# Optimization experiments

Measured on AMD Instinct MI355X. Metric: run time of the kernel, lower is better.

## Reference

```python
import jax, jax.numpy as jnp
import numpy as np

B, T, D = 2, 2048, 2048
H = 16
HD = D // H  # 128


def _rotate_half(x):
    x1, x2 = x[..., :HD // 2], x[..., HD // 2:]
    return jnp.concatenate((-x2, x1), axis=-1)


def setup_inputs() -> dict:
    key = jax.random.key(0)
    ks = jax.random.split(key, 7)
    return {
        "x": jax.random.normal(ks[0], (B, T, D), dtype=jnp.float32),
        "rope_cos": jax.random.uniform(ks[1], (1, 1, T, HD), dtype=jnp.float32),
        "rope_sin": jax.random.uniform(ks[2], (1, 1, T, HD), dtype=jnp.float32),
        "qkv_w": jax.random.normal(ks[3], (3 * D, D), dtype=jnp.float32) * (1.0 / np.sqrt(D)),
        "qkv_b": jax.random.normal(ks[4], (3 * D,), dtype=jnp.float32) * 0.02,
        "out_w": jax.random.normal(ks[5], (D, D), dtype=jnp.float32) * (1.0 / np.sqrt(D)),
        "out_b": jax.random.normal(ks[6], (D,), dtype=jnp.float32) * 0.02,
    }


def reference(x, rope_cos, rope_sin, qkv_w, qkv_b, out_w, out_b):
    bsz, t, d = x.shape
    # fused QKV projection (torch Linear: x @ W.T + b)
    qkv = x @ qkv_w.T + qkv_b                       # [B, T, 3D]
    qkv = qkv.reshape(bsz, t, 3, H, HD).transpose(2, 0, 3, 1, 4)  # [3, B, H, T, HD]
    q, k, v = qkv[0], qkv[1], qkv[2]
    # RoPE
    cos = rope_cos[:, :, :t, :]
    sin = rope_sin[:, :, :t, :]
    q = q * cos + _rotate_half(q) * sin
    k = k * cos + _rotate_half(k) * sin
    # causal SDPA (eval mode -> no dropout)
    scale = 1.0 / np.sqrt(HD)
    scores = jnp.einsum("bhqd,bhkd->bhqk", q, k) * scale
    causal = jnp.tril(jnp.ones((t, t), dtype=bool))
    scores = jnp.where(causal, scores, jnp.finfo(scores.dtype).min)
    attn = jax.nn.softmax(scores, axis=-1)
    out = jnp.einsum("bhqk,bhkd->bhqd", attn, v)    # [B, H, T, HD]
    out = out.transpose(0, 2, 1, 3).reshape(bsz, t, d)
    return out @ out_w.T + out_b
```

## Files before the change

### kernel.cpp

```cpp
#include <hip/hip_runtime.h>

typedef unsigned short u16;
typedef __attribute__((ext_vector_type(8))) short bf16x8;
typedef __attribute__((ext_vector_type(4))) float f32x4;

__device__ __forceinline__ float bf2f(unsigned int u) {
    union { unsigned int i; float f; } x; x.i = u << 16; return x.f;
}
__device__ __forceinline__ u16 f2bf(float f) {
    union { float f; unsigned int i; } x; x.f = f;
    unsigned int r = x.i + 0x7fffu + ((x.i >> 16) & 1u);
    return (u16)(r >> 16);
}

__device__ __forceinline__ void gl2lds16(const u16* g, u16* l) {
    __builtin_amdgcn_global_load_lds(
        (const __attribute__((address_space(1))) unsigned int*)g,
        (__attribute__((address_space(3))) unsigned int*)l, 16, 0, 0);
}

#define NX  8388608
#define NW1 12582912
#define NW2 4194304
__global__ __launch_bounds__(256) void convert_kernel(
    const float* __restrict__ x, const float* __restrict__ w1,
    const float* __restrict__ w2, u16* __restrict__ dst)
{
    const int i = (blockIdx.x * 256 + threadIdx.x) * 4;
    const float* src;
    int off;
    if (i < NX)            { src = x;  off = i; }
    else if (i < NX + NW1) { src = w1; off = i - NX; }
    else                   { src = w2; off = i - NX - NW1; }
    float4 v = *(const float4*)(src + off);
    ushort4 o;
    o.x = f2bf(v.x); o.y = f2bf(v.y); o.z = f2bf(v.z); o.w = f2bf(v.w);
    *(ushort4*)(dst + i) = o;
}

#define NTILES 64
#define BUFSZ  12288

#define GEMM_SETUP(Ag, Bg)                                                    \
    const int tid = threadIdx.x;                                              \
    const int wave = tid >> 6, lane = tid & 63;                               \
    const int l16 = lane & 15, quad = lane >> 4;                              \
    const int wr = wave >> 2, wc = wave & 3;                                  \
    f32x4 acc[4][4];                                                          \
    _Pragma("unroll") for (int mi = 0; mi < 4; ++mi)                          \
        _Pragma("unroll") for (int ni = 0; ni < 4; ++ni)                      \
            acc[mi][ni] = (f32x4){0.f, 0.f, 0.f, 0.f};                        \
    int aoff[4], boff[4];                                                     \
    _Pragma("unroll") for (int mi = 0; mi < 4; ++mi) {                        \
        const int r = wr * 64 + mi * 16 + l16;                                \
        aoff[mi] = r * 32 + ((quad ^ ((r >> 1) & 3)) << 3);                   \
    }                                                                         \
    _Pragma("unroll") for (int ni = 0; ni < 4; ++ni) {                        \
        const int r = (wc >> 1) * 128 + (ni >> 1) * 64 + (wc & 1) * 32        \
                    + (ni & 1) * 16 + l16;                                    \
        boff[ni] = 4096 + r * 32 + ((quad ^ ((r >> 1) & 3)) << 3);            \
    }                                                                         \
    const u16* sbase[3]; int sdst[3];                                         \
    _Pragma("unroll") for (int j = 0; j < 3; ++j) {                           \
        const int c = wave * 3 + j;                                           \
        const int g = lane & 3;                                               \
        int r; const u16* bp; int d;                                          \
        if (c < 8) {                                                          \
            r = c * 16 + (lane >> 2);                                         \
            bp = Ag + (size_t)(m0 + r) * 2048;                                \
            d = c * 512 + lane * 8;                                           \
        } else {                                                              \
            r = (c - 8) * 16 + (lane >> 2);                                   \
            bp = Bg + (size_t)(n0 + r) * 2048;                                \
            d = 4096 + (c - 8) * 512 + lane * 8;                              \
        }                                                                     \
        sbase[j] = bp + ((g ^ ((r >> 1) & 3)) << 3);                          \
        sdst[j] = d;                                                          \
    }                                                                         \
       \
    _Pragma("unroll") for (int pt = 0; pt < 3; ++pt)                          \
        _Pragma("unroll") for (int j = 0; j < 3; ++j)                         \
            gl2lds16(sbase[j] + pt * 32, lds + pt * BUFSZ + sdst[j]);         \
    bf16x8 afr[2][4], bfr[2][4];                                              \
    asm volatile("s_waitcnt vmcnt(6)" ::: "memory");                          \
    __builtin_amdgcn_s_barrier();                                             \
    _Pragma("unroll") for (int mi = 0; mi < 4; ++mi)                          \
        afr[0][mi] = *(const bf16x8*)(lds + aoff[mi]);                        \
    _Pragma("unroll") for (int ni = 0; ni < 4; ++ni)                          \
        bfr[0][ni] = *(const bf16x8*)(lds + boff[ni]);

#define GPH(TT, SLOT, PAR, STG, VMN, RD, LGN)                                 \
    {                                                                         \
        if (STG) {                                                            \
            u16* nb = lds + (((SLOT) + 3) & 3) * BUFSZ;                       \
            _Pragma("unroll") for (int j = 0; j < 3; ++j)                     \
                gl2lds16(sbase[j] + ((TT) + 3) * 32, nb + sdst[j]);           \
        }                                                                     \
        asm volatile("s_waitcnt vmcnt(" #VMN ")" ::: "memory");               \
        __builtin_amdgcn_s_barrier();                                         \
        if (RD) {                                                             \
            const u16* rb = lds + (((SLOT) + 1) & 3) * BUFSZ;                 \
            _Pragma("unroll") for (int mi = 0; mi < 4; ++mi)                  \
                afr[(PAR) ^ 1][mi] = *(const bf16x8*)(rb + aoff[mi]);         \
            _Pragma("unroll") for (int ni = 0; ni < 4; ++ni)                  \
                bfr[(PAR) ^ 1][ni] = *(const bf16x8*)(rb + boff[ni]);         \
        }                                                                     \
        asm volatile("s_waitcnt lgkmcnt(" #LGN ")" ::: "memory");             \
        __builtin_amdgcn_sched_barrier(0);                                    \
        __builtin_amdgcn_s_setprio(1);                                        \
        _Pragma("unroll") for (int mi = 0; mi < 4; ++mi)                      \
            _Pragma("unroll") for (int ni = 0; ni < 4; ++ni)                  \
                acc[mi][ni] = __builtin_amdgcn_mfma_f32_16x16x32_bf16(        \
                    afr[PAR][mi], bfr[PAR][ni], acc[mi][ni], 0, 0, 0);        \
        __builtin_amdgcn_s_setprio(0);                                        \
        __builtin_amdgcn_sched_barrier(0);                                    \
        __builtin_amdgcn_s_barrier();                                         \
    }

#define GEMM_MAIN()                                                           \
    for (int t = 0; t < 15; ++t) {                                            \
        const int T = t * 4;                                                  \
        GPH(T,     0, 0, 1, 6, 1, 8)                                          \
        GPH(T + 1, 1, 1, 1, 6, 1, 8)                                          \
        GPH(T + 2, 2, 0, 1, 6, 1, 8)                                          \
        GPH(T + 3, 3, 1, 1, 6, 1, 8)                                          \
    }                                                                         \
    GPH(60, 0, 0, 1, 6, 1, 8)                                                 \
    GPH(61, 1, 1, 0, 3, 1, 8)                                                 \
    GPH(62, 2, 0, 0, 0, 1, 8)                                                 \
    GPH(63, 3, 1, 0, 0, 0, 0)

__global__ __launch_bounds__(512, 2) void qkv8_kernel(
    const u16* __restrict__ xb, const u16* __restrict__ wb,
    const float* __restrict__ bias, const float* __restrict__ rc,
    const float* __restrict__ rs, u16* __restrict__ Qo,
    u16* __restrict__ Ko, u16* __restrict__ Vo)
{
    __shared__ u16 lds[4 * BUFSZ];
    const int bid = blockIdx.x;
    const int xcd = bid & 7, j = bid >> 3;
    const int m0 = (xcd * 4 + (j & 3)) * 128;
    const int n0 = (j >> 2) * 256;

    GEMM_SETUP(xb, wb)
    GEMM_MAIN()

    const int e  = n0 >> 11;
    const int h  = ((n0 & 2047) >> 7) + (wc >> 1);
    const int hb = n0 + (wc >> 1) * 128;
    const int hq = wc & 1;
    if (e < 2) {
        u16* dst = (e == 0) ? Qo : Ko;
        #pragma unroll
        for (int mi = 0; mi < 4; ++mi) {
            #pragma unroll
            for (int r = 0; r < 4; ++r) {
                const int m = m0 + wr * 64 + mi * 16 + quad * 4 + r;
                const int b = m >> 11, tt = m & 2047;
                u16* drow = dst + ((size_t)(b * 16 + h) * 2048 + tt) * 128;
                const float* crow = rc + tt * 128;
                const float* sr2  = rs + tt * 128;
                #pragma unroll
                for (int p = 0; p < 2; ++p) {
                    const int hd1 = hq * 32 + p * 16 + l16;
                    const int hd2 = hd1 + 64;
                    const float v1 = acc[mi][p][r]     + bias[hb + hd1];
                    const float v2 = acc[mi][p + 2][r] + bias[hb + hd2];
                    drow[hd1] = f2bf(v1 * crow[hd1] - v2 * sr2[hd1]);
                    drow[hd2] = f2bf(v2 * crow[hd2] + v1 * sr2[hd2]);
                }
            }
        }
    } else {
        #pragma unroll
        for (int mi = 0; mi < 4; ++mi) {
            const int mb = m0 + wr * 64 + mi * 16 + quad * 4;
            const int b = mb >> 11, tt = mb & 2047;
            u16* vbase = Vo + (size_t)(b * 16 + h) * 128 * 2048 + tt;
            #pragma unroll
            for (int ni = 0; ni < 4; ++ni) {
                const int hd = (ni >> 1) * 64 + hq * 32 + (ni & 1) * 16 + l16;
                const float bs = bias[hb + hd];
                ushort4 o;
                #pragma unroll
                for (int r = 0; r < 4; ++r)
                    ((u16*)&o)[r] = f2bf(acc[mi][ni][r] + bs);
                *(ushort4*)(vbase + (size_t)hd * 2048) = o;
            }
        }
    }
}

#define KPAD 136
#define VPAD 72
#define PPAD 72

__global__ __launch_bounds__(256) void attn_mfma_kernel(
    const u16* __restrict__ Qi, const u16* __restrict__ Ki,
    const u16* __restrict__ Vg, u16* __restrict__ Oo)
{
    __shared__ u16 Ks[64 * KPAD];
    __shared__ u16 Vt[128 * VPAD];
    __shared__ u16 Ps[4][16 * PPAD];

    const int tid  = threadIdx.x;
    const int wave = tid >> 6, lane = tid & 63;
    const int l16 = lane & 15, quad = lane >> 4;
    const int bh = blockIdx.y;
    const size_t base = (size_t)bh * (2048 * 128);

    const int qtile[2] = { (int)blockIdx.x, 31 - (int)blockIdx.x };

    bf16x8 qf[2][4];
    f32x4 o[2][8];
    float l_i[2][4];
    #pragma unroll
    for (int s = 0; s < 2; ++s) {
        const u16* qp = Qi + base + (size_t)(qtile[s] * 64 + wave * 16 + l16) * 128 + quad * 8;
        #pragma unroll
        for (int c = 0; c < 4; ++c) qf[s][c] = *(const bf16x8*)(qp + c * 32);
        #pragma unroll
        for (int i = 0; i < 8; ++i) o[s][i] = (f32x4){0.f, 0.f, 0.f, 0.f};
        #pragma unroll
        for (int r = 0; r < 4; ++r) l_i[s][r] = 0.f;
    }

    const float scale = 0.08838834764831845f;
    const int ntiles = qtile[1] + 1;

    for (int t = 0; t < ntiles; ++t) {
        const int kt = t * 64;
        __syncthreads();
        {
            const int key = tid >> 2, d0 = (tid & 3) * 32;
            const u16* src = Ki + base + (size_t)(kt + key) * 128 + d0;
            u16* dst = Ks + key * KPAD + d0;
            #pragma unroll
            for (int i = 0; i < 4; ++i)
                *(bf16x8*)(dst + 8 * i) = *(const bf16x8*)(src + 8 * i);
        }
        {
            const int d = tid >> 1, koff = (tid & 1) * 32;
            const u16* src = Vg + ((size_t)bh * 128 + d) * 2048 + kt + koff;
            u16* dst = Vt + d * VPAD + koff;
            #pragma unroll
            for (int i = 0; i < 4; ++i)
                *(bf16x8*)(dst + 8 * i) = *(const bf16x8*)(src + 8 * i);
        }
        __syncthreads();

        const bool act_a = (t <= qtile[0]);

        f32x4 sa[4], sb[4];
        #pragma unroll
        for (int nt = 0; nt < 4; ++nt) {
            sa[nt] = (f32x4){0.f, 0.f, 0.f, 0.f};
            sb[nt] = (f32x4){0.f, 0.f, 0.f, 0.f};
        }
        if (act_a) {
            #pragma unroll
            for (int nt = 0; nt < 4; ++nt)
                #pragma unroll
                for (int c = 0; c < 4; ++c) {
                    bf16x8 kf = *(const bf16x8*)(Ks + (nt * 16 + l16) * KPAD + c * 32 + quad * 8);
                    sb[nt] = __builtin_amdgcn_mfma_f32_16x16x32_bf16(qf[1][c], kf, sb[nt], 0, 0, 0);
                    sa[nt] = __builtin_amdgcn_mfma_f32_16x16x32_bf16(qf[0][c], kf, sa[nt], 0, 0, 0);
                }
        } else {
            #pragma unroll
            for (int nt = 0; nt < 4; ++nt)
                #pragma unroll
                for (int c = 0; c < 4; ++c) {
                    bf16x8 kf = *(const bf16x8*)(Ks + (nt * 16 + l16) * KPAD + c * 32 + quad * 8);
                    sb[nt] = __builtin_amdgcn_mfma_f32_16x16x32_bf16(qf[1][c], kf, sb[nt], 0, 0, 0);
                }
        }

        #pragma unroll
        for (int s = 0; s < 2; ++s) {
            if (s == 0 && !act_a) continue;
            f32x4* sc = (s == 0) ? sa : sb;
            const int qrow = qtile[s] * 64 + wave * 16 + quad * 4;
            const bool diag = (t == qtile[s]);

            #pragma unroll
            for (int nt = 0; nt < 4; ++nt) {
                #pragma unroll
                for (int r = 0; r < 4; ++r) {
                    float v = sc[nt][r] * scale - 11.0f;
                    if (diag) {
                        const int key = kt + nt * 16 + l16;
                        v = (key <= qrow + r) ? v : -1.0e30f;
                    }
                    const float e = __expf(v);
                    sc[nt][r] = e;
                    l_i[s][r] += e;
                }
            }

            u16* pw = Ps[wave];
            #pragma unroll
            for (int nt = 0; nt < 4; ++nt)
                #pragma unroll
                for (int r = 0; r < 4; ++r)
                    pw[(quad * 4 + r) * PPAD + nt * 16 + l16] = f2bf(sc[nt][r]);

            bf16x8 pf0 = *(const bf16x8*)(pw + l16 * PPAD + quad * 8);
            bf16x8 pf1 = *(const bf16x8*)(pw + l16 * PPAD + 32 + quad * 8);

            #pragma unroll
            for (int nt = 0; nt < 8; ++nt) {
                bf16x8 vf0 = *(const bf16x8*)(Vt + (nt * 16 + l16) * VPAD + quad * 8);
                bf16x8 vf1 = *(const bf16x8*)(Vt + (nt * 16 + l16) * VPAD + 32 + quad * 8);
                o[s][nt] = __builtin_amdgcn_mfma_f32_16x16x32_bf16(pf0, vf0, o[s][nt], 0, 0, 0);
                o[s][nt] = __builtin_amdgcn_mfma_f32_16x16x32_bf16(pf1, vf1, o[s][nt], 0, 0, 0);
            }
        }
    }

    const int b = bh >> 4, h = bh & 15;
    #pragma unroll
    for (int s = 0; s < 2; ++s) {
        const int qrow = qtile[s] * 64 + wave * 16 + quad * 4;
        #pragma unroll
        for (int r = 0; r < 4; ++r) {
            float ls = l_i[s][r];
            ls += __shfl_xor(ls, 1, 16);
            ls += __shfl_xor(ls, 2, 16);
            ls += __shfl_xor(ls, 4, 16);
            ls += __shfl_xor(ls, 8, 16);
            const float inv = 1.f / ls;
            u16* orow = Oo + ((size_t)(b * 2048 + qrow + r)) * 2048 + h * 128 + l16;
            #pragma unroll
            for (int nt = 0; nt < 8; ++nt)
                orow[nt * 16] = f2bf(o[s][nt][r] * inv);
        }
    }
}

__global__ __launch_bounds__(512, 2) void proj8_kernel(
    const u16* __restrict__ A, const u16* __restrict__ wb,
    const float* __restrict__ bias, float* __restrict__ out)
{
    __shared__ u16 lds[4 * BUFSZ];
    const int bid = blockIdx.x;
    const int xcd = bid & 7, j = bid >> 3;
    const int m0 = (xcd * 4 + (j & 3)) * 128;
    const int n0 = (j >> 2) * 256;

    GEMM_SETUP(A, wb)
    GEMM_MAIN()

    #pragma unroll
    for (int mi = 0; mi < 4; ++mi) {
        #pragma unroll
        for (int r = 0; r < 4; ++r) {
            const int m = m0 + wr * 64 + mi * 16 + quad * 4 + r;
            float* orow = out + (size_t)m * 2048;
            #pragma unroll
            for (int ni = 0; ni < 4; ++ni) {
                const int n = n0 + (wc >> 1) * 128 + (ni >> 1) * 64
                            + (wc & 1) * 32 + (ni & 1) * 16 + l16;
                orow[n] = acc[mi][ni][r] + bias[n];
            }
        }
    }
}

extern "C" void kernel_launch(void* const* d_in, const int* in_sizes, int n_in,
                              void* d_out, int out_size, void* d_ws, size_t ws_size,
                              hipStream_t stream) {
    const float* x     = (const float*)d_in[0];
    const float* rcos  = (const float*)d_in[1];
    const float* rsin  = (const float*)d_in[2];
    const float* qkv_w = (const float*)d_in[3];
    const float* qkv_b = (const float*)d_in[4];
    const float* out_w = (const float*)d_in[5];
    const float* out_b = (const float*)d_in[6];
    float* out = (float*)d_out;

    const size_t NE = (size_t)2 * 16 * 2048 * 128;
    u16* Q      = (u16*)d_ws;
    u16* K      = Q + NE;
    u16* V      = K + NE;
    u16* xb     = V + NE;
    u16* O      = xb;
    u16* qkv_wb = xb + NX;
    u16* out_wb = qkv_wb + NW1;

    convert_kernel<<<dim3((NX + NW1 + NW2) / 1024), 256, 0, stream>>>(
        x, qkv_w, out_w, xb);
    qkv8_kernel<<<dim3(768), 512, 0, stream>>>(
        xb, qkv_wb, qkv_b, rcos, rsin, Q, K, V);
    attn_mfma_kernel<<<dim3(16, 32), 256, 0, stream>>>(Q, K, V, O);
    proj8_kernel<<<dim3(256), 512, 0, stream>>>(O, out_wb, out_b, out);
}
```

Baseline: 394.8 us.

## Double-buffer attention K/V tiles via direct global-to-LDS loads with XOR swizzle

The attention kernel now streams K and V tiles into two LDS buffers using global_load_lds, prefetching the next tile while the current one is computed. This replaces synchronous register-staged copies and their two barriers per tile. Padded LDS layouts are replaced with an XOR swizzle to avoid bank conflicts. The branch that skipped the QK MFMAs for the inactive low q-tile is removed, so that work is always computed and then discarded. LDS use roughly doubles, and correctness now depends on manual vmcnt/lgkmcnt waits.

```diff
diff --git a/kernel.cpp b/kernel.cpp
--- a/kernel.cpp
+++ b/kernel.cpp
@@ -191,16 +191,14 @@
     }
 }
 
-#define KPAD 136
-#define VPAD 72
 #define PPAD 72
 
 __global__ __launch_bounds__(256) void attn_mfma_kernel(
     const u16* __restrict__ Qi, const u16* __restrict__ Ki,
     const u16* __restrict__ Vg, u16* __restrict__ Oo)
 {
-    __shared__ u16 Ks[64 * KPAD];
-    __shared__ u16 Vt[128 * VPAD];
+    __shared__ u16 Ks[2][64 * 128];
+    __shared__ u16 Vt[2][128 * 64];
     __shared__ u16 Ps[4][16 * PPAD];
 
     const int tid  = threadIdx.x;
@@ -225,30 +223,52 @@
         for (int r = 0; r < 4; ++r) l_i[s][r] = 0.f;
     }
 
+    const u16* kb = Ki + base;
+    const u16* vb = Vg + (size_t)bh * 128 * 2048;
+
+    int ksrc[4], vsrc0[4], kdst[4], vdst[4];
+    #pragma unroll
+    for (int i = 0; i < 4; ++i) {
+        const int G = i * 256 + tid;
+        const int kr = G >> 4, kg = (G & 15) ^ (kr & 7);
+        const int vr = G >> 3, vg = (G & 7)  ^ (vr & 7);
+        ksrc[i]  = kr * 128 + (kg << 3);
+        vsrc0[i] = vr * 2048 + (vg << 3);
+        kdst[i] = G * 8;
+        vdst[i] = G * 8;
+    }
+
     const float scale = 0.08838834764831845f;
     const int ntiles = qtile[1] + 1;
 
+    #pragma unroll
+    for (int i = 0; i < 4; ++i) {
+        gl2lds16(kb + ksrc[i], Ks[0] + kdst[i]);
+        gl2lds16(vb + vsrc0[i], Vt[0] + vdst[i]);
+    }
+    asm volatile("s_waitcnt vmcnt(8)" ::: "memory");
+
     for (int t = 0; t < ntiles; ++t) {
         const int kt = t * 64;
-        __syncthreads();
-        {
-            const int key = tid >> 2, d0 = (tid & 3) * 32;
-            const u16* src = Ki + base + (size_t)(kt + key) * 128 + d0;
-            u16* dst = Ks + key * KPAD + d0;
-            #pragma unroll
-            for (int i = 0; i < 4; ++i)
-                *(bf16x8*)(dst + 8 * i) = *(const bf16x8*)(src + 8 * i);
-        }
-        {
-            const int d = tid >> 1, koff = (tid & 1) * 32;
-            const u16* src = Vg + ((size_t)bh * 128 + d) * 2048 + kt + koff;
-            u16* dst = Vt + d * VPAD + koff;
-            #pragma unroll
-            for (int i = 0; i < 4; ++i)
-                *(bf16x8*)(dst + 8 * i) = *(const bf16x8*)(src + 8 * i);
-        }
-        __syncthreads();
-
+        const int cb = t & 1;
+
+        if (t + 1 < ntiles) {
+            const int kt1 = kt + 64;
+            u16* ksd = Ks[cb ^ 1];
+            u16* vsd = Vt[cb ^ 1];
+            #pragma unroll
+            for (int i = 0; i < 4; ++i) {
+                gl2lds16(kb + (size_t)kt1 * 128 + ksrc[i], ksd + kdst[i]);
+                gl2lds16(vb + kt1 + vsrc0[i], vsd + vdst[i]);
+            }
+            asm volatile("s_waitcnt vmcnt(8)" ::: "memory");
+        } else {
+            asm volatile("s_waitcnt vmcnt(0)" ::: "memory");
+        }
+        __builtin_amdgcn_s_barrier();
+
+        const u16* KsC = Ks[cb];
+        const u16* VtC = Vt[cb];
         const bool act_a = (t <= qtile[0]);
 
         f32x4 sa[4], sb[4];
@@ -256,24 +276,14 @@
         for (int nt = 0; nt < 4; ++nt) {
             sa[nt] = (f32x4){0.f, 0.f, 0.f, 0.f};
             sb[nt] = (f32x4){0.f, 0.f, 0.f, 0.f};
-        }
-        if (act_a) {
-            #pragma unroll
-            for (int nt = 0; nt < 4; ++nt)
-                #pragma unroll
-                for (int c = 0; c < 4; ++c) {
-                    bf16x8 kf = *(const bf16x8*)(Ks + (nt * 16 + l16) * KPAD + c * 32 + quad * 8);
-                    sb[nt] = __builtin_amdgcn_mfma_f32_16x16x32_bf16(qf[1][c], kf, sb[nt], 0, 0, 0);
-                    sa[nt] = __builtin_amdgcn_mfma_f32_16x16x32_bf16(qf[0][c], kf, sa[nt], 0, 0, 0);
-                }
-        } else {
-            #pragma unroll
-            for (int nt = 0; nt < 4; ++nt)
-                #pragma unroll
-                for (int c = 0; c < 4; ++c) {
-                    bf16x8 kf = *(const bf16x8*)(Ks + (nt * 16 + l16) * KPAD + c * 32 + quad * 8);
-                    sb[nt] = __builtin_amdgcn_mfma_f32_16x16x32_bf16(qf[1][c], kf, sb[nt], 0, 0, 0);
-                }
+            const int kr2 = nt * 16 + l16;
+            #pragma unroll
+            for (int c = 0; c < 4; ++c) {
+                bf16x8 kf = *(const bf16x8*)(
+                    KsC + kr2 * 128 + ((((c << 2) + quad) ^ (kr2 & 7)) << 3));
+                sb[nt] = __builtin_amdgcn_mfma_f32_16x16x32_bf16(qf[1][c], kf, sb[nt], 0, 0, 0);
+                sa[nt] = __builtin_amdgcn_mfma_f32_16x16x32_bf16(qf[0][c], kf, sa[nt], 0, 0, 0);
+            }
         }
 
         #pragma unroll
@@ -310,12 +320,18 @@
 
             #pragma unroll
             for (int nt = 0; nt < 8; ++nt) {
-                bf16x8 vf0 = *(const bf16x8*)(Vt + (nt * 16 + l16) * VPAD + quad * 8);
-                bf16x8 vf1 = *(const bf16x8*)(Vt + (nt * 16 + l16) * VPAD + 32 + quad * 8);
+                const int vr2 = nt * 16 + l16;
+                bf16x8 vf0 = *(const bf16x8*)(
+                    VtC + vr2 * 64 + ((quad ^ (vr2 & 7)) << 3));
+                bf16x8 vf1 = *(const bf16x8*)(
+                    VtC + vr2 * 64 + (((quad + 4) ^ (vr2 & 7)) << 3));
                 o[s][nt] = __builtin_amdgcn_mfma_f32_16x16x32_bf16(pf0, vf0, o[s][nt], 0, 0, 0);
                 o[s][nt] = __builtin_amdgcn_mfma_f32_16x16x32_bf16(pf1, vf1, o[s][nt], 0, 0, 0);
             }
         }
+
+        asm volatile("s_waitcnt lgkmcnt(0)" ::: "memory");
+        __builtin_amdgcn_s_barrier();
     }
 
     const int b = bh >> 4, h = bh & 15;
```

Result: faster. 381.6 us (-3.3%).
